# Kernel tuning notes

Measured on AMD Instinct MI355X. Metric: run time of the kernel, lower is better.

Reference implementation:

```python
import jax, jax.numpy as jnp
import numpy as np

PATCH = 4
WINDOW = 4
MAX_ROUNDS = 4
MIN_ROUNDS = 2
LAMBDA_P = 0.2
TOPK = 8


def _ln(x, g, b, eps=1e-5):
    m = x.mean(-1, keepdims=True)
    v = ((x - m) ** 2).mean(-1, keepdims=True)
    return (x - m) / jnp.sqrt(v + eps) * g + b


def _mlp(x, w1, b1, w2, b2):
    # Linear -> exact GELU -> Linear (matches nn.GELU default)
    return jax.nn.gelu(x @ w1 + b1, approximate=False) @ w2 + b2


def setup_inputs() -> dict:
    key = jax.random.key(0)
    ks = jax.random.split(key, 24)
    B, T, D, V = 16, 4096, 256, 256
    s = 0.02
    w = lambda i, shape: jax.random.normal(ks[i], shape, jnp.float32) * s
    z = lambda *shape: jnp.zeros(shape, jnp.float32)
    o = lambda *shape: jnp.ones(shape, jnp.float32)
    return {
        'x': jax.random.randint(ks[0], (B, T), 0, V),
        'emb': w(1, (V, D)), 'pos': w(2, (PATCH, D)),
        'gru_wih': w(3, (D, 3 * D)), 'gru_whh': w(4, (D, 3 * D)),
        'gru_bih': z(3 * D), 'gru_bhh': z(3 * D),
        'ln_p_g': o(D), 'ln_p_b': z(D),
        'sum_w': w(5, (D, D)), 'sum_b': z(D),
        'msg_w1': w(6, (2 * D, D)), 'msg_b1': z(D), 'msg_w2': w(7, (D, D)), 'msg_b2': z(D),
        'upd_w1': w(8, (2 * D, D)), 'upd_b1': z(D), 'upd_w2': w(9, (D, D)), 'upd_b2': z(D),
        'halt_w': w(10, (D, 1)), 'halt_b': z(1),
        'ln_mp_g': o(D), 'ln_mp_b': z(D),
        'q_w': w(11, (D, D)), 'q_b': z(D),
        'k_w': w(12, (D, D)), 'k_b': z(D),
        'v_w': w(13, (D, D)), 'v_b': z(D),
        'o_w': w(14, (D, D)), 'o_b': z(D),
        'bc_w': w(15, (D, D)), 'bc_b': z(D),
        'ln_f_g': o(D), 'ln_f_b': z(D),
        'head_w': w(16, (D, V)),
    }


def reference(x, emb, pos, gru_wih, gru_whh, gru_bih, gru_bhh, ln_p_g, ln_p_b,
              sum_w, sum_b, msg_w1, msg_b1, msg_w2, msg_b2, upd_w1, upd_b1,
              upd_w2, upd_b2, halt_w, halt_b, ln_mp_g, ln_mp_b, q_w, q_b,
              k_w, k_b, v_w, v_b, o_w, o_b, bc_w, bc_b, ln_f_g, ln_f_b, head_w):
    B, T = x.shape
    D = emb.shape[1]
    Np = T // PATCH  # T is divisible by PATCH for these shapes (no pad needed)

    # --- GRU patch processor over B*Np sequences of length PATCH ---
    tok = x.reshape(B * Np, PATCH)
    hseq = emb[tok] + pos[None]  # [BN, P, D]

    def gru_step(h, xt):
        gi = xt @ gru_wih + gru_bih
        gh = h @ gru_whh + gru_bhh
        ir, iz, inn = jnp.split(gi, 3, -1)
        hr, hz, hn = jnp.split(gh, 3, -1)
        r = jax.nn.sigmoid(ir + hr)
        zz = jax.nn.sigmoid(iz + hz)
        n = jnp.tanh(inn + r * hn)
        h = (1 - zz) * n + zz * h
        return h, h

    h0 = jnp.zeros((B * Np, D), hseq.dtype)
    _, gout = jax.lax.scan(gru_step, h0, jnp.swapaxes(hseq, 0, 1))
    local = _ln(jnp.swapaxes(gout, 0, 1), ln_p_g, ln_p_b).reshape(B, Np, PATCH, D)
    summaries = local.mean(2) @ sum_w + sum_b  # [B, Np, D]

    # --- Local message passing with ACT-style halting (fixed MAX_ROUNDS) ---
    h = summaries
    remaining = jnp.ones((B, Np, 1), h.dtype)
    out_mp = jnp.zeros_like(h)
    kl = jnp.zeros((), h.dtype)
    for step in range(MAX_ROUNDS):
        padded = jnp.pad(h, ((0, 0), (WINDOW, 0), (0, 0)))
        # neighbors: self plus previous WINDOW patches -> [B, Np, W+1, D]
        neigh = jnp.stack([padded[:, WINDOW - w:WINDOW - w + Np] for w in range(WINDOW + 1)], axis=2)
        self_exp = jnp.broadcast_to(h[:, :, None, :], neigh.shape)
        msgs = _mlp(jnp.concatenate([self_exp, neigh], -1), msg_w1, msg_b1, msg_w2, msg_b2).mean(2)
        h = _ln(h + _mlp(jnp.concatenate([h, msgs], -1), upd_w1, upd_b1, upd_w2, upd_b2), ln_mp_g, ln_mp_b)
        if step < MIN_ROUNDS:
            hp = jnp.zeros((B, Np, 1), h.dtype)
        else:
            hp = jax.nn.sigmoid(h.mean(1, keepdims=True) @ halt_w + halt_b)  # [B,1,1]
            hp = jnp.broadcast_to(hp, (B, Np, 1))
        if step == MAX_ROUNDS - 1:
            hp = jnp.ones_like(hp)
        out_mp = out_mp + remaining * hp * h
        remaining = remaining * (1 - hp)
        p_geom = LAMBDA_P * (1 - LAMBDA_P) ** step
        # F.kl_div(log(mean+eps), log(p_geom), log_target=True) = p*(log p - log(mean+eps))
        kl = kl + p_geom * (np.log(p_geom) - jnp.log(hp.mean() + 1e-8))
    kl = kl / MAX_ROUNDS

    # --- Sparse top-k causal retrieval ---
    q = out_mp @ q_w + q_b
    kk = out_mp @ k_w + k_b
    v = out_mp @ v_w + v_b
    scores = jnp.einsum('bnd,bmd->bnm', q, kk) / np.sqrt(D).astype(np.float32)
    causal = jnp.tril(jnp.ones((Np, Np), bool))
    neg = jnp.asarray(-jnp.inf, scores.dtype)
    scores = jnp.where(causal[None], scores, neg)
    vals, idx = jax.lax.top_k(scores, TOPK)  # [B, Np, k]
    bi = jnp.arange(B)[:, None, None]
    ni = jnp.arange(Np)[None, :, None]
    sparse = jnp.full_like(scores, neg).at[bi, ni, idx].set(vals)
    attn = jax.nn.softmax(sparse, axis=-1)
    retrieved = jnp.einsum('bnm,bmd->bnd', attn, v) @ o_w + o_b

    # --- Broadcast back to tokens and project ---
    combined = out_mp + retrieved
    broad = combined @ bc_w + bc_b
    final = (local + broad[:, :, None, :]).reshape(B, Np * PATCH, D)[:, :T]
    logits = _ln(final, ln_f_g, ln_f_b) @ head_w
    return logits, kl
```

## Files before the change

kernel.cpp:

```cpp
#include <hip/hip_runtime.h>
#include <math.h>


typedef __bf16 bf16_t;
typedef bf16_t bf16x8 __attribute__((ext_vector_type(8)));
typedef bf16_t bf16x4 __attribute__((ext_vector_type(4)));
typedef float f32x4 __attribute__((ext_vector_type(4)));

#define GF_BIAS 1
#define GF_GELU 4
#define GF_RES 8
#define GF_F32OUT 32

__device__ __forceinline__ float gelu_exact(float x) {
  return 0.5f * x * (1.0f + erff(x * 0.7071067811865475f));
}

__device__ __forceinline__ float sigm(float x) { return 1.f / (1.f + expf(-x)); }

__device__ __forceinline__ float wave_sum(float v) {
#pragma unroll
  for (int o = 32; o; o >>= 1) v += __shfl_xor(v, o, 64);
  return v;
}

__device__ __forceinline__ void gload16(const void* g, void* l) {
  __builtin_amdgcn_global_load_lds(
      (const __attribute__((address_space(1))) void*)g,
      (__attribute__((address_space(3))) void*)l, 16, 0, 0);
}

__device__ __forceinline__ unsigned long long skey(float s, int m) {
  unsigned u = __float_as_uint(s);
  u ^= (u & 0x80000000u) ? 0xFFFFFFFFu : 0x80000000u;
  return ((unsigned long long)u << 32) | (unsigned)(0x7FFFFFFF - m);
}

template<int FLAGS>
__global__ __launch_bounds__(256)
void gemm_bt(const bf16_t* __restrict__ A, const bf16_t* __restrict__ Bt,
             void* __restrict__ Cv, const float* __restrict__ bias,
             const bf16_t* __restrict__ res,
             int lda, int ldb, int ldc, int ldr)
{
  __shared__ __align__(16) bf16_t As[128][64];
  __shared__ __align__(16) bf16_t Bs[128][64];
  const int m0 = blockIdx.x * 128, n0 = blockIdx.y * 128;
  const int tid = threadIdx.x, lane = tid & 63, wave = tid >> 6;
  const int wm = (wave >> 1) << 6, wn = (wave & 1) << 6;
  const int lr = lane & 15, lg = lane >> 4;
  const int cx = lane & 7;

  const int srow = wave * 32 + (lane >> 3);
  const int scol = (((lane & 7) ^ ((lane >> 3) & 7)) * 8);
  const bf16_t* ga = A  + (long long)(m0 + srow) * lda + scol;
  const bf16_t* gb = Bt + (long long)(n0 + srow) * ldb + scol;
  char* lA = (char*)(&As[srow][0]) + (lane & 7) * 16;
  char* lB = (char*)(&Bs[srow][0]) + (lane & 7) * 16;

  f32x4 acc[4][4] = {};

#pragma unroll
  for (int kt = 0; kt < 4; kt++) {
    const int ko = kt * 64;
#pragma unroll
    for (int q = 0; q < 4; q++) {
      gload16(ga + (long long)q * 8 * lda + ko, lA + q * 1024);
      gload16(gb + (long long)q * 8 * ldb + ko, lB + q * 1024);
    }
    __syncthreads();
#pragma unroll
    for (int kk = 0; kk < 2; kk++) {
      const int co = ((kk * 4 + lg) ^ cx) << 4;
      bf16x8 af[4], bfv[4];
#pragma unroll
      for (int i = 0; i < 4; i++)
        af[i]  = *(const bf16x8*)((char*)As + (wm + i * 16 + lr) * 128 + co);
#pragma unroll
      for (int j = 0; j < 4; j++)
        bfv[j] = *(const bf16x8*)((char*)Bs + (wn + j * 16 + lr) * 128 + co);
#pragma unroll
      for (int i = 0; i < 4; i++)
#pragma unroll
        for (int j = 0; j < 4; j++)
          acc[i][j] = __builtin_amdgcn_mfma_f32_16x16x32_bf16(af[i], bfv[j], acc[i][j], 0, 0, 0);
    }
    if (kt < 3) __syncthreads();
  }

#pragma unroll
  for (int i = 0; i < 4; i++) {
#pragma unroll
    for (int j = 0; j < 4; j++) {
      const int col = n0 + wn + j * 16 + lr;
      const float bval = (FLAGS & GF_BIAS) ? bias[col] : 0.f;
#pragma unroll
      for (int e = 0; e < 4; e++) {
        const int row = m0 + wm + i * 16 + lg * 4 + e;
        float v = acc[i][j][e] + bval;
        if (FLAGS & GF_RES) v += (float)res[(long long)row * ldr + col];
        if (FLAGS & GF_GELU) v = gelu_exact(v);
        const long long ci = (long long)row * ldc + col;
        if (FLAGS & GF_F32OUT) ((float*)Cv)[ci] = v;
        else                   ((bf16_t*)Cv)[ci] = (bf16_t)v;
      }
    }
  }
}

template<int FLAGS>
__global__ __launch_bounds__(256)
void gemm64(const bf16_t* __restrict__ A, const bf16_t* __restrict__ Bt,
            void* __restrict__ Cv, const float* __restrict__ bias,
            const bf16_t* __restrict__ res,
            int lda, int ldb, int ldc, int ldr)
{
  __shared__ __align__(16) bf16_t As[64][64];
  __shared__ __align__(16) bf16_t Bs[64][64];
  const int m0 = blockIdx.x * 64, n0 = blockIdx.y * 64;
  const int tid = threadIdx.x, lane = tid & 63, wave = tid >> 6;
  const int wm = (wave >> 1) * 32, wn = (wave & 1) * 32;
  const int lr = lane & 15, lg = lane >> 4;
  const int cx = lane & 7;

  const int srow = tid >> 3;
  const int scol = (((tid & 7) ^ (srow & 7)) * 8);
  const bf16_t* ga = A  + (long long)(m0 + srow) * lda + scol;
  const bf16_t* gb = Bt + (long long)(n0 + srow) * ldb + scol;
  char* lA = (char*)As + tid * 16;
  char* lB = (char*)Bs + tid * 16;

  f32x4 acc[2][2] = {};

#pragma unroll
  for (int kt = 0; kt < 4; kt++) {
    const int ko = kt * 64;
    gload16(ga + ko, lA);
    gload16(ga + 32LL * lda + ko, lA + 4096);
    gload16(gb + ko, lB);
    gload16(gb + 32LL * ldb + ko, lB + 4096);
    __syncthreads();
#pragma unroll
    for (int kk = 0; kk < 2; kk++) {
      const int co = ((kk * 4 + lg) ^ cx) << 4;
      bf16x8 af[2], bfv[2];
#pragma unroll
      for (int i = 0; i < 2; i++)
        af[i]  = *(const bf16x8*)((char*)As + (wm + i * 16 + lr) * 128 + co);
#pragma unroll
      for (int j = 0; j < 2; j++)
        bfv[j] = *(const bf16x8*)((char*)Bs + (wn + j * 16 + lr) * 128 + co);
#pragma unroll
      for (int i = 0; i < 2; i++)
#pragma unroll
        for (int j = 0; j < 2; j++)
          acc[i][j] = __builtin_amdgcn_mfma_f32_16x16x32_bf16(af[i], bfv[j], acc[i][j], 0, 0, 0);
    }
    if (kt < 3) __syncthreads();
  }

#pragma unroll
  for (int i = 0; i < 2; i++) {
#pragma unroll
    for (int j = 0; j < 2; j++) {
      const int col = n0 + wn + j * 16 + lr;
      const float bval = (FLAGS & GF_BIAS) ? bias[col] : 0.f;
#pragma unroll
      for (int e = 0; e < 4; e++) {
        const int row = m0 + wm + i * 16 + lg * 4 + e;
        float v = acc[i][j][e] + bval;
        if (FLAGS & GF_RES) v += (float)res[(long long)row * ldr + col];
        if (FLAGS & GF_GELU) v = gelu_exact(v);
        const long long ci = (long long)row * ldc + col;
        if (FLAGS & GF_F32OUT) ((float*)Cv)[ci] = v;
        else                   ((bf16_t*)Cv)[ci] = (bf16_t)v;
      }
    }
  }
}

template<int MODE>
__global__ __launch_bounds__(256)
void gemm_ln(const bf16_t* __restrict__ A, const bf16_t* __restrict__ Bt,
             bf16_t* __restrict__ C, const float* __restrict__ bias,
             const float* __restrict__ g, const float* __restrict__ bvec,
             bf16_t* __restrict__ OUTMP, const float* __restrict__ HP)
{
  __shared__ __align__(16) bf16_t As[64][64];
  __shared__ __align__(16) bf16_t Bs[256][64];
  __shared__ float redsum[4][64];
  __shared__ float redsq[4][64];
  const int m0 = blockIdx.x * 64;
  const int tid = threadIdx.x, lane = tid & 63, w = tid >> 6;
  const int lr = lane & 15, lg = lane >> 4, cx = lane & 7;

  f32x4 acc[4][4] = {};

#pragma unroll
  for (int kt = 0; kt < 4; kt++) {
    const int ko = kt * 64;
    {
      int cid = tid, r = cid >> 3, c = cid & 7;
      gload16(A + (long long)(m0 + r) * 256 + ko + ((c ^ (r & 7)) * 8), (char*)As + cid * 16);
      cid = tid + 256; r = cid >> 3; c = cid & 7;
      gload16(A + (long long)(m0 + r) * 256 + ko + ((c ^ (r & 7)) * 8), (char*)As + cid * 16);
    }
#pragma unroll
    for (int it = 0; it < 8; it++) {
      const int cid = it * 256 + tid, r = cid >> 3, c = cid & 7;
      gload16(Bt + (long long)r * 256 + ko + ((c ^ (r & 7)) * 8), (char*)Bs + cid * 16);
    }
    __syncthreads();
#pragma unroll
    for (int kk = 0; kk < 2; kk++) {
      const int co = ((kk * 4 + lg) ^ cx) << 4;
      bf16x8 af[4], bfv[4];
#pragma unroll
      for (int i = 0; i < 4; i++)
        af[i]  = *(const bf16x8*)((char*)As + (i * 16 + lr) * 128 + co);
#pragma unroll
      for (int j = 0; j < 4; j++)
        bfv[j] = *(const bf16x8*)((char*)Bs + (w * 64 + j * 16 + lr) * 128 + co);
#pragma unroll
      for (int i = 0; i < 4; i++)
#pragma unroll
        for (int j = 0; j < 4; j++)
          acc[i][j] = __builtin_amdgcn_mfma_f32_16x16x32_bf16(af[i], bfv[j], acc[i][j], 0, 0, 0);
    }
    if (kt < 3) __syncthreads();
  }

  float v[4][4][4];
  float rs[4][4], rq[4][4];
#pragma unroll
  for (int i = 0; i < 4; i++) {
#pragma unroll
    for (int e = 0; e < 4; e++) { rs[i][e] = 0.f; rq[i][e] = 0.f; }
  }
#pragma unroll
  for (int i = 0; i < 4; i++) {
#pragma unroll
    for (int j = 0; j < 4; j++) {
      const int col = w * 64 + j * 16 + lr;
      const float bval = bias[col];
#pragma unroll
      for (int e = 0; e < 4; e++) {
        const long long rg = m0 + i * 16 + lg * 4 + e;
        const float val = acc[i][j][e] + bval + (float)C[rg * 256 + col];
        v[i][j][e] = val;
        rs[i][e] += val;
        rq[i][e] += val * val;
      }
    }
  }
#pragma unroll
  for (int off = 1; off < 16; off <<= 1) {
#pragma unroll
    for (int i = 0; i < 4; i++)
#pragma unroll
      for (int e = 0; e < 4; e++) {
        rs[i][e] += __shfl_xor(rs[i][e], off, 64);
        rq[i][e] += __shfl_xor(rq[i][e], off, 64);
      }
  }
  if (lr == 0) {
#pragma unroll
    for (int i = 0; i < 4; i++)
#pragma unroll
      for (int e = 0; e < 4; e++) {
        redsum[w][i * 16 + lg * 4 + e] = rs[i][e];
        redsq[w][i * 16 + lg * 4 + e]  = rq[i][e];
      }
  }
  __syncthreads();
  float mean[4][4], rstd[4][4];
#pragma unroll
  for (int i = 0; i < 4; i++) {
#pragma unroll
    for (int e = 0; e < 4; e++) {
      const int r = i * 16 + lg * 4 + e;
      const float S = redsum[0][r] + redsum[1][r] + redsum[2][r] + redsum[3][r];
      const float Q = redsq[0][r] + redsq[1][r] + redsq[2][r] + redsq[3][r];
      const float m = S * (1.f / 256.f);
      float var = Q * (1.f / 256.f) - m * m;
      if (var < 0.f) var = 0.f;
      mean[i][e] = m;
      rstd[i][e] = rsqrtf(var + 1e-5f);
    }
  }
#pragma unroll
  for (int i = 0; i < 4; i++) {
#pragma unroll
    for (int j = 0; j < 4; j++) {
      const int col = w * 64 + j * 16 + lr;
      const float gg = g[col], bb = bvec[col];
#pragma unroll
      for (int e = 0; e < 4; e++) {
        const long long rg = m0 + i * 16 + lg * 4 + e;
        const float y = (v[i][j][e] - mean[i][e]) * rstd[i][e] * gg + bb;
        if (MODE == 0) {
          C[rg * 256 + col] = (bf16_t)y;
        } else {
          const float rem = 1.f - HP[(int)(rg >> 10)];
          OUTMP[rg * 256 + col] = (bf16_t)((float)OUTMP[rg * 256 + col] + rem * y);
        }
      }
    }
  }
}

__global__ __launch_bounds__(256)
void k_fatopk(const bf16_t* __restrict__ QKV, bf16_t* __restrict__ O) {
  __shared__ unsigned long long cand[4][16][8];
  __shared__ float wrow[16][8];
  __shared__ int   irow[16][8];
  const int b = blockIdx.y;
  const int tid = threadIdx.x;
  const int wid = tid >> 6;
  const int lane = tid & 63;
  const int lr = lane & 15, lg = lane >> 4;
  const bf16_t* Qp = QKV + (long long)b * (1024LL * 768);
  const bf16_t* Kp = Qp + 256;
  const bf16_t* Vp = Qp + 512;

  for (int half = 0; half < 2; half++) {
    const int qw = (half == 0) ? (int)blockIdx.x : 63 - (int)blockIdx.x;
    const int q0 = qw * 16;
    const int qrow = q0 + lr;

    bf16x8 bq[8];
#pragma unroll
    for (int s = 0; s < 8; s++)
      bq[s] = *(const bf16x8*)(Qp + (long long)qrow * 768 + s * 32 + lg * 8);

    unsigned long long kv[8] = {0ull, 0ull, 0ull, 0ull, 0ull, 0ull, 0ull, 0ull};

#define INS8(KEY) {                                                     \
    const unsigned long long k_ = (KEY);                                \
    if (k_ > kv[7]) {                                                   \
      kv[7] = k_;                                                       \
      _Pragma("unroll")                                                 \
      for (int j_ = 7; j_ > 0; j_--)                                    \
        if (kv[j_] > kv[j_-1]) {                                        \
          const unsigned long long t_ = kv[j_];                         \
          kv[j_] = kv[j_-1]; kv[j_-1] = t_;                             \
        }                                                               \
    }                                                                   \
  }

    const int klim = qw + 1;
    for (int kt = wid; kt < klim; kt += 4) {
      const bf16_t* ka = Kp + (long long)(kt * 16 + lr) * 768 + lg * 8;
      bf16x8 af[8];
#pragma unroll
      for (int s = 0; s < 8; s++) af[s] = *(const bf16x8*)(ka + s * 32);
      f32x4 a0 = {}, a1 = {};
#pragma unroll
      for (int s = 0; s < 8; s += 2) {
        a0 = __builtin_amdgcn_mfma_f32_16x16x32_bf16(af[s],     bq[s],     a0, 0, 0, 0);
        a1 = __builtin_amdgcn_mfma_f32_16x16x32_bf16(af[s + 1], bq[s + 1], a1, 0, 0, 0);
      }
#pragma unroll
      for (int e = 0; e < 4; e++) {
        const int m = kt * 16 + lg * 4 + e;
        if (m <= qrow) INS8(skey((a0[e] + a1[e]) * 0.0625f, m));
      }
    }
#undef INS8

#pragma unroll
    for (int r = 0; r < 8; r++) {
      unsigned long long mk = kv[0];
      unsigned long long ok = __shfl_xor(mk, 16, 64); if (ok > mk) mk = ok;
      ok = __shfl_xor(mk, 32, 64); if (ok > mk) mk = ok;
      if (lg == 0) cand[wid][lr][r] = mk;
      if (kv[0] == mk && mk != 0ull) {
#pragma unroll
        for (int j = 0; j < 7; j++) kv[j] = kv[j + 1];
        kv[7] = 0ull;
      }
    }
    __syncthreads();

    if (wid == 0) {
      unsigned long long kv2[8];
#pragma unroll
      for (int j = 0; j < 8; j++) kv2[j] = cand[lg][lr][j];
      float wv[8]; int wi[8];
#pragma unroll
      for (int r = 0; r < 8; r++) {
        unsigned long long mk = kv2[0];
        unsigned long long ok = __shfl_xor(mk, 16, 64); if (ok > mk) mk = ok;
        ok = __shfl_xor(mk, 32, 64); if (ok > mk) mk = ok;
        if (mk != 0ull) {
          unsigned hi = (unsigned)(mk >> 32);
          hi ^= (hi & 0x80000000u) ? 0x80000000u : 0xFFFFFFFFu;
          wv[r] = __uint_as_float(hi);
          wi[r] = 0x7FFFFFFF - (int)(unsigned)(mk & 0xFFFFFFFFu);
        } else {
          wv[r] = 0.f; wi[r] = -1;
        }
        if (kv2[0] == mk && mk != 0ull) {
#pragma unroll
          for (int j = 0; j < 7; j++) kv2[j] = kv2[j + 1];
          kv2[7] = 0ull;
        }
      }
      const float mx = wv[0];
      float w8[8]; float den = 0.f;
#pragma unroll
      for (int j = 0; j < 8; j++) {
        w8[j] = (wi[j] >= 0) ? expf(wv[j] - mx) : 0.f;
        den += w8[j];
      }
      const float inv = 1.f / den;
      if (lg == 0) {
#pragma unroll
        for (int j = 0; j < 8; j++) {
          wrow[lr][j] = w8[j] * inv;
          irow[lr][j] = wi[j];
        }
      }
    }
    __syncthreads();

    const int rr = wid * 4 + lg;
    const int c0 = (lane & 15) * 16;
    f32x4 av[4] = {};
#pragma unroll
    for (int j = 0; j < 8; j++) {
      const int idx = irow[rr][j];
      if (idx >= 0) {
        const float wj = wrow[rr][j];
        const bf16_t* vr = Vp + (long long)idx * 768 + c0;
        const bf16x8 v0 = *(const bf16x8*)vr;
        const bf16x8 v1 = *(const bf16x8*)(vr + 8);
#pragma unroll
        for (int e = 0; e < 4; e++) {
          av[0][e] = fmaf(wj, (float)v0[e],     av[0][e]);
          av[1][e] = fmaf(wj, (float)v0[4 + e], av[1][e]);
          av[2][e] = fmaf(wj, (float)v1[e],     av[2][e]);
          av[3][e] = fmaf(wj, (float)v1[4 + e], av[3][e]);
        }
      }
    }
    bf16_t* op = O + ((long long)b * 1024 + q0 + rr) * 256 + c0;
    bf16x8 o0, o1;
#pragma unroll
    for (int e = 0; e < 4; e++) {
      o0[e] = (bf16_t)av[0][e]; o0[4 + e] = (bf16_t)av[1][e];
      o1[e] = (bf16_t)av[2][e]; o1[4 + e] = (bf16_t)av[3][e];
    }
    *(bf16x8*)op = o0;
    *(bf16x8*)(op + 8) = o1;
    if (half == 0) __syncthreads();
  }
}

struct TD { const float* src; bf16_t* dst; int N; int k0; int ld; };
struct PrepArgs {
  TD d[16];
  const float* emb; const float* pos; bf16_t* XE;
  const float* msg_b1; const float* msg_b2; const float* upd_w1; const float* upd_b1;
  const float* q_b; const float* k_b; const float* v_b;
  float* BIAS3; float* QKVB;
};

__global__ __launch_bounds__(256) void k_prep(PrepArgs pa) {
  const int y = blockIdx.y, x = blockIdx.x, d = threadIdx.x;
  if (y < 16) {
    TD t = pa.d[y];
    if (x >= t.N) return;
    if (t.k0 < 0) t.dst[(long long)x * 256 + d] = (bf16_t)t.src[(long long)x * t.ld + d];
    else          t.dst[(long long)x * 256 + d] = (bf16_t)t.src[(long long)(t.k0 + d) * t.ld + x];
  } else if (y == 16) {
    const int p = x >> 8, v = x & 255;
    pa.XE[(long long)x * 256 + d] = (bf16_t)(pa.emb[v * 256 + d] + pa.pos[p * 256 + d]);
  } else {
    if      (x == 0) pa.BIAS3[d] = pa.msg_b1[d];
    else if (x == 1) pa.BIAS3[256 + d] = 0.f;
    else if (x == 2) {
      float acc = pa.upd_b1[d];
      for (int k = 0; k < 256; k++) acc += pa.msg_b2[k] * pa.upd_w1[(long long)(256 + k) * 256 + d];
      pa.BIAS3[512 + d] = acc;
    }
    else if (x == 3) pa.QKVB[d] = pa.q_b[d];
    else if (x == 4) pa.QKVB[256 + d] = pa.k_b[d];
    else if (x == 5) pa.QKVB[512 + d] = pa.v_b[d];
  }
}

__global__ __launch_bounds__(64)
void k_gru_gate(const int* __restrict__ x, const bf16_t* __restrict__ gitab,
                const bf16_t* __restrict__ GH, const float* __restrict__ bhh,
                bf16_t* __restrict__ H, bf16_t* __restrict__ LOC, int t)
{
  const int s = blockIdx.x, lane = threadIdx.x, d0 = lane * 4;
  const int v = x[s * 4 + t];
  const bf16_t* gi = gitab + (long long)(t * 256 + v) * 768;
  const bf16x4 g_r = *(const bf16x4*)(gi + d0);
  const bf16x4 g_z = *(const bf16x4*)(gi + 256 + d0);
  const bf16x4 g_n = *(const bf16x4*)(gi + 512 + d0);
  float hr[4], hz[4], hn[4], hp[4];
  if (t == 0) {
#pragma unroll
    for (int e = 0; e < 4; e++) {
      hr[e] = bhh[d0 + e]; hz[e] = bhh[256 + d0 + e]; hn[e] = bhh[512 + d0 + e];
      hp[e] = 0.f;
    }
  } else {
    const bf16_t* gh = GH + (long long)s * 768;
    const bf16x4 a = *(const bf16x4*)(gh + d0);
    const bf16x4 b4 = *(const bf16x4*)(gh + 256 + d0);
    const bf16x4 c4 = *(const bf16x4*)(gh + 512 + d0);
    const bf16x4 hv = *(const bf16x4*)(H + (long long)s * 256 + d0);
#pragma unroll
    for (int e = 0; e < 4; e++) { hr[e] = a[e]; hz[e] = b4[e]; hn[e] = c4[e]; hp[e] = hv[e]; }
  }
  bf16x4 ho;
#pragma unroll
  for (int e = 0; e < 4; e++) {
    const float r = sigm((float)g_r[e] + hr[e]);
    const float zz = sigm((float)g_z[e] + hz[e]);
    const float nn = tanhf((float)g_n[e] + r * hn[e]);
    ho[e] = (bf16_t)((1.f - zz) * nn + zz * hp[e]);
  }
  *(bf16x4*)(H + (long long)s * 256 + d0) = ho;
  *(bf16x4*)(LOC + ((long long)s * 4 + t) * 256 + d0) = ho;
}

__global__ __launch_bounds__(64)
void k_ln(const bf16_t* __restrict__ X, const bf16_t* __restrict__ ADD, int addmode,
          bf16_t* __restrict__ OUT, const float* __restrict__ g,
          const float* __restrict__ b)
{
  const long long r = blockIdx.x;
  const int d0 = threadIdx.x * 4;
  const bf16x4 xv = *(const bf16x4*)(X + r * 256 + d0);
  float xf[4];
#pragma unroll
  for (int e = 0; e < 4; e++) xf[e] = (float)xv[e];
  if (addmode == 1) {
    const bf16x4 av = *(const bf16x4*)(ADD + r * 256 + d0);
#pragma unroll
    for (int e = 0; e < 4; e++) xf[e] += (float)av[e];
  } else if (addmode == 2) {
    const bf16x4 av = *(const bf16x4*)(ADD + (r >> 2) * 256 + d0);
#pragma unroll
    for (int e = 0; e < 4; e++) xf[e] += (float)av[e];
  }
  const float mean = wave_sum(xf[0] + xf[1] + xf[2] + xf[3]) * (1.f / 256.f);
  float q = 0.f;
#pragma unroll
  for (int e = 0; e < 4; e++) { const float dx = xf[e] - mean; q += dx * dx; }
  const float rstd = rsqrtf(wave_sum(q) * (1.f / 256.f) + 1e-5f);
  const float4 gv = *(const float4*)(g + d0);
  const float4 bv = *(const float4*)(b + d0);
  const float gg[4] = {gv.x, gv.y, gv.z, gv.w};
  const float bb[4] = {bv.x, bv.y, bv.z, bv.w};
  bf16x4 ov;
#pragma unroll
  for (int e = 0; e < 4; e++) ov[e] = (bf16_t)((xf[e] - mean) * rstd * gg[e] + bb[e]);
  *(bf16x4*)(OUT + r * 256 + d0) = ov;
}

__global__ __launch_bounds__(64)
void k_lnp4(bf16_t* __restrict__ LOC, bf16_t* __restrict__ SUMB,
            const float* __restrict__ g, const float* __restrict__ b)
{
  const long long s = blockIdx.x;
  const int d0 = threadIdx.x * 4;
  const float4 gv = *(const float4*)(g + d0);
  const float4 bv = *(const float4*)(b + d0);
  const float gg[4] = {gv.x, gv.y, gv.z, gv.w};
  const float bb[4] = {bv.x, bv.y, bv.z, bv.w};
  float accd[4] = {0.f, 0.f, 0.f, 0.f};
#pragma unroll
  for (int t = 0; t < 4; t++) {
    bf16_t* row = LOC + (s * 4 + t) * 256 + d0;
    const bf16x4 xv = *(const bf16x4*)row;
    float xf[4];
#pragma unroll
    for (int e = 0; e < 4; e++) xf[e] = (float)xv[e];
    const float mean = wave_sum(xf[0] + xf[1] + xf[2] + xf[3]) * (1.f / 256.f);
    float q = 0.f;
#pragma unroll
    for (int e = 0; e < 4; e++) { const float dx = xf[e] - mean; q += dx * dx; }
    const float rstd = rsqrtf(wave_sum(q) * (1.f / 256.f) + 1e-5f);
    bf16x4 ov;
#pragma unroll
    for (int e = 0; e < 4; e++) {
      const float y = (xf[e] - mean) * rstd * gg[e] + bb[e];
      ov[e] = (bf16_t)y;
      accd[e] += y;
    }
    *(bf16x4*)row = ov;
  }
  bf16x4 sv;
#pragma unroll
  for (int e = 0; e < 4; e++) sv[e] = (bf16_t)(accd[e] * 0.25f);
  *(bf16x4*)(SUMB + s * 256 + d0) = sv;
}

__global__ __launch_bounds__(64)
void k_gelumix(const bf16_t* __restrict__ A3, bf16_t* __restrict__ G)
{
  const long long s = blockIdx.x;
  const int n = (int)(s & 1023);
  const int d0 = threadIdx.x * 4;
  const bf16x4 av = *(const bf16x4*)(A3 + s * 768 + d0);
  float a[4];
#pragma unroll
  for (int e = 0; e < 4; e++) a[e] = (float)av[e];
  float acc[4] = {0.f, 0.f, 0.f, 0.f};
  const bf16_t* bbase = A3 + s * 768 + 256 + d0;
#pragma unroll
  for (int w = 0; w <= 4; w++) {
    if (n >= w) {
      const bf16x4 bn = *(const bf16x4*)(bbase - (long long)w * 768);
#pragma unroll
      for (int e = 0; e < 4; e++) acc[e] += gelu_exact(a[e] + (float)bn[e]);
    } else {
#pragma unroll
      for (int e = 0; e < 4; e++) acc[e] += gelu_exact(a[e]);
    }
  }
  bf16x4 ov;
#pragma unroll
  for (int e = 0; e < 4; e++) ov[e] = (bf16_t)(acc[e] * 0.2f);
  *(bf16x4*)(G + s * 256 + d0) = ov;
}

__global__ __launch_bounds__(64)
void k_halt1(const bf16_t* __restrict__ Hm, float* __restrict__ PS) {
  const int c = blockIdx.x, b = blockIdx.y, d0 = threadIdx.x * 4;
  float acc[4] = {0.f, 0.f, 0.f, 0.f};
  const bf16_t* base = Hm + ((long long)b * 1024 + c * 32) * 256 + d0;
#pragma unroll 4
  for (int n = 0; n < 32; n++) {
    const bf16x4 hv = *(const bf16x4*)(base + (long long)n * 256);
#pragma unroll
    for (int e = 0; e < 4; e++) acc[e] += (float)hv[e];
  }
  float4 o4; o4.x = acc[0]; o4.y = acc[1]; o4.z = acc[2]; o4.w = acc[3];
  *(float4*)(PS + ((long long)b * 32 + c) * 256 + d0) = o4;
}

__global__ __launch_bounds__(1024)
void k_halt2kl(const float* __restrict__ PS, const float* __restrict__ hw,
               const float* __restrict__ hb, float* __restrict__ HP,
               float* __restrict__ out) {
  __shared__ float sh[16];
  const int b = threadIdx.x >> 6, lane = threadIdx.x & 63, d0 = lane * 4;
  float acc[4] = {0.f, 0.f, 0.f, 0.f};
  for (int c = 0; c < 32; c++) {
    const float4 p4 = *(const float4*)(PS + ((long long)b * 32 + c) * 256 + d0);
    acc[0] += p4.x; acc[1] += p4.y; acc[2] += p4.z; acc[3] += p4.w;
  }
  const float4 w4 = *(const float4*)(hw + d0);
  float val = (acc[0] * w4.x + acc[1] * w4.y + acc[2] * w4.z + acc[3] * w4.w) * (1.f / 1024.f);
  val = wave_sum(val);
  if (lane == 0) {
    const float hp = sigm(val + hb[0]);
    HP[b] = hp;
    sh[b] = hp;
  }
  __syncthreads();
  if (threadIdx.x == 0) {
    float s = 0.f;
    for (int bb = 0; bb < 16; bb++) s += sh[bb];
    const float hpm = s * (1.f / 16.f);
    const float l8 = logf(1e-8f);
    const float p0 = 0.2f, p1 = 0.16f, p2 = 0.128f, p3 = 0.1024f;
    const float kl = p0 * (logf(p0) - l8)
                   + p1 * (logf(p1) - l8)
                   + p2 * (logf(p2) - logf(hpm + 1e-8f))
                   + p3 * (logf(p3) - logf(1.f + 1e-8f));
    out[0] = kl * 0.25f;
  }
}

__global__ __launch_bounds__(64)
void k_outmp(const bf16_t* __restrict__ Hm, const float* __restrict__ HP,
             bf16_t* __restrict__ O, int acc) {
  const long long s = blockIdx.x;
  const int d0 = threadIdx.x * 4;
  const int b = (int)(s >> 10);
  const float hp = HP[b];
  const bf16x4 hv = *(const bf16x4*)(Hm + s * 256 + d0);
  bf16x4 ov;
  if (acc) {
    const bf16x4 pv = *(const bf16x4*)(O + s * 256 + d0);
#pragma unroll
    for (int e = 0; e < 4; e++) ov[e] = (bf16_t)((float)pv[e] + (1.f - hp) * (float)hv[e]);
  } else {
#pragma unroll
    for (int e = 0; e < 4; e++) ov[e] = (bf16_t)(hp * (float)hv[e]);
  }
  *(bf16x4*)(O + s * 256 + d0) = ov;
}

extern "C" void kernel_launch(void* const* d_in, const int* in_sizes, int n_in,
                              void* d_out, int out_size, void* d_ws, size_t ws_size,
                              hipStream_t stream) {
  (void)in_sizes; (void)n_in; (void)ws_size;
  const int*   x      = (const int*)d_in[0];
  const float* emb    = (const float*)d_in[1];
  const float* pos    = (const float*)d_in[2];
  const float* wih    = (const float*)d_in[3];
  const float* whh    = (const float*)d_in[4];
  const float* bih    = (const float*)d_in[5];
  const float* bhh    = (const float*)d_in[6];
  const float* lnp_g  = (const float*)d_in[7];
  const float* lnp_b  = (const float*)d_in[8];
  const float* sum_w  = (const float*)d_in[9];
  const float* sum_b  = (const float*)d_in[10];
  const float* msg_w1 = (const float*)d_in[11];
  const float* msg_b1 = (const float*)d_in[12];
  const float* msg_w2 = (const float*)d_in[13];
  const float* msg_b2 = (const float*)d_in[14];
  const float* upd_w1 = (const float*)d_in[15];
  const float* upd_b1 = (const float*)d_in[16];
  const float* upd_w2 = (const float*)d_in[17];
  const float* upd_b2 = (const float*)d_in[18];
  const float* halt_w = (const float*)d_in[19];
  const float* halt_b = (const float*)d_in[20];
  const float* lnm_g  = (const float*)d_in[21];
  const float* lnm_b  = (const float*)d_in[22];
  const float* q_b    = (const float*)d_in[24];
  const float* k_b    = (const float*)d_in[26];
  const float* v_b    = (const float*)d_in[28];
  const float* o_b    = (const float*)d_in[30];
  const float* bc_b   = (const float*)d_in[32];
  const float* lnf_g  = (const float*)d_in[33];
  const float* lnf_b  = (const float*)d_in[34];

  char* base = (char*)d_ws;
  size_t off = 0;
  auto alloc = [&](size_t bytes) -> void* {
    void* p = (void*)(base + off);
    off += (bytes + 255) & ~(size_t)255;
    return p;
  };
  const size_t SL2 = 16384ull * 256 * 2;
  bf16_t* WIHT  = (bf16_t*)alloc(768 * 256 * 2);
  bf16_t* WHHT  = (bf16_t*)alloc(768 * 256 * 2);
  bf16_t* SUMT  = (bf16_t*)alloc(256 * 256 * 2);
  bf16_t* MW    = (bf16_t*)alloc(768 * 256 * 2);
  bf16_t* W2T   = (bf16_t*)alloc(256 * 256 * 2);
  bf16_t* W2NT  = (bf16_t*)alloc(256 * 256 * 2);
  bf16_t* UW1MT = (bf16_t*)alloc(256 * 256 * 2);
  bf16_t* UW2T  = (bf16_t*)alloc(256 * 256 * 2);
  bf16_t* WCB   = (bf16_t*)alloc(256 * 256 * 2);
  bf16_t* QKVW  = (bf16_t*)alloc(768 * 256 * 2);
  bf16_t* OT    = (bf16_t*)alloc(256 * 256 * 2);
  bf16_t* BCT   = (bf16_t*)alloc(256 * 256 * 2);
  bf16_t* HEADT = (bf16_t*)alloc(256 * 256 * 2);
  float*  BIAS3 = (float*)alloc(768 * 4);
  float*  QKVB  = (float*)alloc(768 * 4);
  bf16_t* XE    = (bf16_t*)alloc(1024ull * 256 * 2);
  bf16_t* GITAB = (bf16_t*)alloc(1024ull * 768 * 2);
  bf16_t* LOCb  = (bf16_t*)alloc(65536ull * 256 * 2);

  char*   SCR   = (char*)alloc(16ull * 1024 * 1024 * 4);
  bf16_t* GH    = (bf16_t*)SCR;
  bf16_t* H     = (bf16_t*)(SCR + 25165824);
  bf16_t* SUMB  = (bf16_t*)(SCR + 33554432);
  bf16_t* A3    = (bf16_t*)(SCR + 41943040);

  bf16_t* HMP   = (bf16_t*)alloc(SL2);
  bf16_t* G     = (bf16_t*)alloc(SL2);
  bf16_t* BROAD = (bf16_t*)alloc(SL2);
  bf16_t* UB    = (bf16_t*)alloc(SL2);
  bf16_t* U2B   = (bf16_t*)alloc(SL2);
  bf16_t* OUTMP = (bf16_t*)alloc(SL2);
  bf16_t* QKV   = (bf16_t*)alloc(16384ull * 768 * 2);
  float*  PS    = (float*)alloc(512ull * 256 * 4);
  float*  HP    = (float*)alloc(64);
  bf16_t* ATT   = UB;
  bf16_t* COMB  = U2B;
  float*  out   = (float*)d_out;
  float*  klout = out + (out_size - 1);

  PrepArgs pa;
  pa.d[0]  = { wih,                    WIHT,            768, 0,   768 };
  pa.d[1]  = { whh,                    WHHT,            768, 0,   768 };
  pa.d[2]  = { sum_w,                  SUMT,            256, 0,   256 };
  pa.d[3]  = { msg_w1,                 MW,              256, 0,   256 };
  pa.d[4]  = { msg_w1,                 MW + 256 * 256,  256, 256, 256 };
  pa.d[5]  = { upd_w1,                 MW + 512 * 256,  256, 0,   256 };
  pa.d[6]  = { msg_w2,                 W2T,             256, 0,   256 };
  pa.d[7]  = { upd_w1,                 UW1MT,           256, 256, 256 };
  pa.d[8]  = { upd_w2,                 UW2T,            256, 0,   256 };
  pa.d[9]  = { (const float*)d_in[23], QKVW,            256, 0,   256 };
  pa.d[10] = { (const float*)d_in[25], QKVW + 256*256,  256, 0,   256 };
  pa.d[11] = { (const float*)d_in[27], QKVW + 512*256,  256, 0,   256 };
  pa.d[12] = { (const float*)d_in[29], OT,              256, 0,   256 };
  pa.d[13] = { (const float*)d_in[31], BCT,             256, 0,   256 };
  pa.d[14] = { (const float*)d_in[35], HEADT,           256, 0,   256 };
  pa.d[15] = { msg_w2,                 W2NT,            256, -1,  256 };
  pa.emb = emb; pa.pos = pos; pa.XE = XE;
  pa.msg_b1 = msg_b1; pa.msg_b2 = msg_b2; pa.upd_w1 = upd_w1; pa.upd_b1 = upd_b1;
  pa.q_b = q_b; pa.k_b = k_b; pa.v_b = v_b;
  pa.BIAS3 = BIAS3; pa.QKVB = QKVB;
  k_prep<<<dim3(1024, 18), 256, 0, stream>>>(pa);

  gemm64<0><<<dim3(4, 4), 256, 0, stream>>>(
      UW1MT, W2NT, WCB, nullptr, nullptr, 256, 256, 256, 0);

  gemm64<GF_BIAS><<<dim3(16, 12), 256, 0, stream>>>(
      XE, WIHT, GITAB, bih, nullptr, 256, 256, 768, 0);

  k_gru_gate<<<16384, 64, 0, stream>>>(x, GITAB, GH, bhh, H, LOCb, 0);
  for (int t = 1; t < 4; t++) {
    gemm_bt<GF_BIAS><<<dim3(128, 6), 256, 0, stream>>>(
        H, WHHT, GH, bhh, nullptr, 256, 256, 768, 0);
    k_gru_gate<<<16384, 64, 0, stream>>>(x, GITAB, GH, bhh, H, LOCb, t);
  }

  k_lnp4<<<16384, 64, 0, stream>>>(LOCb, SUMB, lnp_g, lnp_b);
  gemm64<GF_BIAS><<<dim3(256, 4), 256, 0, stream>>>(
      SUMB, SUMT, HMP, sum_b, nullptr, 256, 256, 256, 0);

  for (int step = 0; step < 4; step++) {
    gemm_bt<GF_BIAS><<<dim3(128, 6), 256, 0, stream>>>(
        HMP, MW, A3, BIAS3, nullptr, 256, 256, 768, 0);
    k_gelumix<<<16384, 64, 0, stream>>>(A3, G);
    gemm64<GF_RES | GF_GELU><<<dim3(256, 4), 256, 0, stream>>>(
        G, WCB, UB, nullptr, A3 + 512, 256, 256, 256, 768);
    if (step == 3) {
      gemm_ln<1><<<256, 256, 0, stream>>>(
          UB, UW2T, HMP, upd_b2, lnm_g, lnm_b, OUTMP, HP);
    } else {
      gemm_ln<0><<<256, 256, 0, stream>>>(
          UB, UW2T, HMP, upd_b2, lnm_g, lnm_b, nullptr, nullptr);
      if (step == 2) {
        k_halt1<<<dim3(32, 16), 64, 0, stream>>>(HMP, PS);
        k_halt2kl<<<1, 1024, 0, stream>>>(PS, halt_w, halt_b, HP, klout);
        k_outmp<<<16384, 64, 0, stream>>>(HMP, HP, OUTMP, 0);
      }
    }
  }

  gemm_bt<GF_BIAS><<<dim3(128, 6), 256, 0, stream>>>(
      OUTMP, QKVW, QKV, QKVB, nullptr, 256, 256, 768, 0);
  k_fatopk<<<dim3(32, 16), 256, 0, stream>>>(QKV, ATT);
  gemm64<GF_BIAS | GF_RES><<<dim3(256, 4), 256, 0, stream>>>(
      ATT, OT, COMB, o_b, OUTMP, 256, 256, 256, 256);
  gemm64<GF_BIAS><<<dim3(256, 4), 256, 0, stream>>>(
      COMB, BCT, BROAD, bc_b, nullptr, 256, 256, 256, 0);

  k_ln<<<65536, 64, 0, stream>>>(LOCb, BROAD, 2, LOCb, lnf_g, lnf_b);
  gemm_bt<GF_F32OUT><<<dim3(512, 2), 256, 0, stream>>>(
      LOCb, HEADT, out, nullptr, nullptr, 256, 256, 256, 0);
}
```

Before: 470.2 us.

## Split topk blocks per query tile, pair key tiles, pack rows per block

```diff
diff --git a/kernel.cpp b/kernel.cpp
--- a/kernel.cpp
+++ b/kernel.cpp
@@ -315,6 +315,7 @@
   __shared__ float wrow[16][8];
   __shared__ int   irow[16][8];
   const int b = blockIdx.y;
+  const int qw = (int)((blockIdx.x + ((unsigned)(b * 21) & 63u)) & 63u);
   const int tid = threadIdx.x;
   const int wid = tid >> 6;
   const int lane = tid & 63;
@@ -322,18 +323,15 @@
   const bf16_t* Qp = QKV + (long long)b * (1024LL * 768);
   const bf16_t* Kp = Qp + 256;
   const bf16_t* Vp = Qp + 512;
-
-  for (int half = 0; half < 2; half++) {
-    const int qw = (half == 0) ? (int)blockIdx.x : 63 - (int)blockIdx.x;
-    const int q0 = qw * 16;
-    const int qrow = q0 + lr;
-
-    bf16x8 bq[8];
-#pragma unroll
-    for (int s = 0; s < 8; s++)
-      bq[s] = *(const bf16x8*)(Qp + (long long)qrow * 768 + s * 32 + lg * 8);
-
-    unsigned long long kv[8] = {0ull, 0ull, 0ull, 0ull, 0ull, 0ull, 0ull, 0ull};
+  const int q0 = qw * 16;
+  const int qrow = q0 + lr;
+
+  bf16x8 bq[8];
+#pragma unroll
+  for (int s = 0; s < 8; s++)
+    bq[s] = *(const bf16x8*)(Qp + (long long)qrow * 768 + s * 32 + lg * 8);
+
+  unsigned long long kv[8] = {0ull, 0ull, 0ull, 0ull, 0ull, 0ull, 0ull, 0ull};
 
 #define INS8(KEY) {                                                     \
     const unsigned long long k_ = (KEY);                                \
@@ -348,113 +346,127 @@
     }                                                                   \
   }
 
-    const int klim = qw + 1;
-    for (int kt = wid; kt < klim; kt += 4) {
-      const bf16_t* ka = Kp + (long long)(kt * 16 + lr) * 768 + lg * 8;
-      bf16x8 af[8];
-#pragma unroll
-      for (int s = 0; s < 8; s++) af[s] = *(const bf16x8*)(ka + s * 32);
-      f32x4 a0 = {}, a1 = {};
-#pragma unroll
-      for (int s = 0; s < 8; s += 2) {
-        a0 = __builtin_amdgcn_mfma_f32_16x16x32_bf16(af[s],     bq[s],     a0, 0, 0, 0);
-        a1 = __builtin_amdgcn_mfma_f32_16x16x32_bf16(af[s + 1], bq[s + 1], a1, 0, 0, 0);
-      }
+  const int klim = qw + 1;
+  for (int base = wid * 2; base < klim; base += 8) {
+    const bool hasB = (base + 1 < klim);
+    const int ktB = hasB ? base + 1 : base;
+    const bf16_t* ka = Kp + (long long)(base * 16 + lr) * 768 + lg * 8;
+    const bf16_t* kb = Kp + (long long)(ktB * 16 + lr) * 768 + lg * 8;
+    bf16x8 afA[8], afB[8];
+#pragma unroll
+    for (int s = 0; s < 8; s++) afA[s] = *(const bf16x8*)(ka + s * 32);
+#pragma unroll
+    for (int s = 0; s < 8; s++) afB[s] = *(const bf16x8*)(kb + s * 32);
+    f32x4 a0 = {}, a1 = {}, b0 = {}, b1 = {};
+    __builtin_amdgcn_s_setprio(1);
+#pragma unroll
+    for (int s = 0; s < 8; s += 2) {
+      a0 = __builtin_amdgcn_mfma_f32_16x16x32_bf16(afA[s],     bq[s],     a0, 0, 0, 0);
+      a1 = __builtin_amdgcn_mfma_f32_16x16x32_bf16(afA[s + 1], bq[s + 1], a1, 0, 0, 0);
+      b0 = __builtin_amdgcn_mfma_f32_16x16x32_bf16(afB[s],     bq[s],     b0, 0, 0, 0);
+      b1 = __builtin_amdgcn_mfma_f32_16x16x32_bf16(afB[s + 1], bq[s + 1], b1, 0, 0, 0);
+    }
+    __builtin_amdgcn_s_setprio(0);
+#pragma unroll
+    for (int e = 0; e < 4; e++) {
+      const int m = base * 16 + lg * 4 + e;
+      if (m <= qrow) INS8(skey((a0[e] + a1[e]) * 0.0625f, m));
+    }
+    if (hasB) {
 #pragma unroll
       for (int e = 0; e < 4; e++) {
-        const int m = kt * 16 + lg * 4 + e;
-        if (m <= qrow) INS8(skey((a0[e] + a1[e]) * 0.0625f, m));
-      }
-    }
+        const int m = ktB * 16 + lg * 4 + e;
+        if (m <= qrow) INS8(skey((b0[e] + b1[e]) * 0.0625f, m));
+      }
+    }
+  }
 #undef INS8
 
 #pragma unroll
+  for (int r = 0; r < 8; r++) {
+    unsigned long long mk = kv[0];
+    unsigned long long ok = __shfl_xor(mk, 16, 64); if (ok > mk) mk = ok;
+    ok = __shfl_xor(mk, 32, 64); if (ok > mk) mk = ok;
+    if (lg == 0) cand[wid][lr][r] = mk;
+    if (kv[0] == mk && mk != 0ull) {
+#pragma unroll
+      for (int j = 0; j < 7; j++) kv[j] = kv[j + 1];
+      kv[7] = 0ull;
+    }
+  }
+  __syncthreads();
+
+  if (wid == 0) {
+    unsigned long long kv2[8];
+#pragma unroll
+    for (int j = 0; j < 8; j++) kv2[j] = cand[lg][lr][j];
+    float wv[8]; int wi[8];
+#pragma unroll
     for (int r = 0; r < 8; r++) {
-      unsigned long long mk = kv[0];
+      unsigned long long mk = kv2[0];
       unsigned long long ok = __shfl_xor(mk, 16, 64); if (ok > mk) mk = ok;
       ok = __shfl_xor(mk, 32, 64); if (ok > mk) mk = ok;
-      if (lg == 0) cand[wid][lr][r] = mk;
-      if (kv[0] == mk && mk != 0ull) {
-#pragma unroll
-        for (int j = 0; j < 7; j++) kv[j] = kv[j + 1];
-        kv[7] = 0ull;
-      }
-    }
-    __syncthreads();
-
-    if (wid == 0) {
-      unsigned long long kv2[8];
-#pragma unroll
-      for (int j = 0; j < 8; j++) kv2[j] = cand[lg][lr][j];
-      float wv[8]; int wi[8];
-#pragma unroll
-      for (int r = 0; r < 8; r++) {
-        unsigned long long mk = kv2[0];
-        unsigned long long ok = __shfl_xor(mk, 16, 64); if (ok > mk) mk = ok;
-        ok = __shfl_xor(mk, 32, 64); if (ok > mk) mk = ok;
-        if (mk != 0ull) {
-          unsigned hi = (unsigned)(mk >> 32);
-          hi ^= (hi & 0x80000000u) ? 0x80000000u : 0xFFFFFFFFu;
-          wv[r] = __uint_as_float(hi);
-          wi[r] = 0x7FFFFFFF - (int)(unsigned)(mk & 0xFFFFFFFFu);
-        } else {
-          wv[r] = 0.f; wi[r] = -1;
-        }
-        if (kv2[0] == mk && mk != 0ull) {
-#pragma unroll
-          for (int j = 0; j < 7; j++) kv2[j] = kv2[j + 1];
-          kv2[7] = 0ull;
-        }
-      }
-      const float mx = wv[0];
-      float w8[8]; float den = 0.f;
+      if (mk != 0ull) {
+        unsigned hi = (unsigned)(mk >> 32);
+        hi ^= (hi & 0x80000000u) ? 0x80000000u : 0xFFFFFFFFu;
+        wv[r] = __uint_as_float(hi);
+        wi[r] = 0x7FFFFFFF - (int)(unsigned)(mk & 0xFFFFFFFFu);
+      } else {
+        wv[r] = 0.f; wi[r] = -1;
+      }
+      if (kv2[0] == mk && mk != 0ull) {
+#pragma unroll
+        for (int j = 0; j < 7; j++) kv2[j] = kv2[j + 1];
+        kv2[7] = 0ull;
+      }
+    }
+    const float mx = wv[0];
+    float w8[8]; float den = 0.f;
+#pragma unroll
+    for (int j = 0; j < 8; j++) {
+      w8[j] = (wi[j] >= 0) ? expf(wv[j] - mx) : 0.f;
+      den += w8[j];
+    }
+    const float inv = 1.f / den;
+    if (lg == 0) {
 #pragma unroll
       for (int j = 0; j < 8; j++) {
-        w8[j] = (wi[j] >= 0) ? expf(wv[j] - mx) : 0.f;
-        den += w8[j];
-      }
-      const float inv = 1.f / den;
-      if (lg == 0) {
-#pragma unroll
-        for (int j = 0; j < 8; j++) {
-          wrow[lr][j] = w8[j] * inv;
-          irow[lr][j] = wi[j];
-        }
-      }
-    }
-    __syncthreads();
-
-    const int rr = wid * 4 + lg;
-    const int c0 = (lane & 15) * 16;
-    f32x4 av[4] = {};
-#pragma unroll
-    for (int j = 0; j < 8; j++) {
-      const int idx = irow[rr][j];
-      if (idx >= 0) {
-        const float wj = wrow[rr][j];
-        const bf16_t* vr = Vp + (long long)idx * 768 + c0;
-        const bf16x8 v0 = *(const bf16x8*)vr;
-        const bf16x8 v1 = *(const bf16x8*)(vr + 8);
-#pragma unroll
-        for (int e = 0; e < 4; e++) {
-          av[0][e] = fmaf(wj, (float)v0[e],     av[0][e]);
-          av[1][e] = fmaf(wj, (float)v0[4 + e], av[1][e]);
-          av[2][e] = fmaf(wj, (float)v1[e],     av[2][e]);
-          av[3][e] = fmaf(wj, (float)v1[4 + e], av[3][e]);
-        }
-      }
-    }
-    bf16_t* op = O + ((long long)b * 1024 + q0 + rr) * 256 + c0;
-    bf16x8 o0, o1;
-#pragma unroll
-    for (int e = 0; e < 4; e++) {
-      o0[e] = (bf16_t)av[0][e]; o0[4 + e] = (bf16_t)av[1][e];
-      o1[e] = (bf16_t)av[2][e]; o1[4 + e] = (bf16_t)av[3][e];
-    }
-    *(bf16x8*)op = o0;
-    *(bf16x8*)(op + 8) = o1;
-    if (half == 0) __syncthreads();
-  }
+        wrow[lr][j] = w8[j] * inv;
+        irow[lr][j] = wi[j];
+      }
+    }
+  }
+  __syncthreads();
+
+  const int rr = wid * 4 + lg;
+  const int c0 = (lane & 15) * 16;
+  f32x4 av[4] = {};
+#pragma unroll
+  for (int j = 0; j < 8; j++) {
+    const int idx = irow[rr][j];
+    if (idx >= 0) {
+      const float wj = wrow[rr][j];
+      const bf16_t* vr = Vp + (long long)idx * 768 + c0;
+      const bf16x8 v0 = *(const bf16x8*)vr;
+      const bf16x8 v1 = *(const bf16x8*)(vr + 8);
+#pragma unroll
+      for (int e = 0; e < 4; e++) {
+        av[0][e] = fmaf(wj, (float)v0[e],     av[0][e]);
+        av[1][e] = fmaf(wj, (float)v0[4 + e], av[1][e]);
+        av[2][e] = fmaf(wj, (float)v1[e],     av[2][e]);
+        av[3][e] = fmaf(wj, (float)v1[4 + e], av[3][e]);
+      }
+    }
+  }
+  bf16_t* op = O + ((long long)b * 1024 + q0 + rr) * 256 + c0;
+  bf16x8 o0, o1;
+#pragma unroll
+  for (int e = 0; e < 4; e++) {
+    o0[e] = (bf16_t)av[0][e]; o0[4 + e] = (bf16_t)av[1][e];
+    o1[e] = (bf16_t)av[2][e]; o1[4 + e] = (bf16_t)av[3][e];
+  }
+  *(bf16x8*)op = o0;
+  *(bf16x8*)(op + 8) = o1;
 }
 
 struct TD { const float* src; bf16_t* dst; int N; int k0; int ld; };
@@ -490,12 +502,13 @@
   }
 }
 
-__global__ __launch_bounds__(64)
+__global__ __launch_bounds__(256)
 void k_gru_gate(const int* __restrict__ x, const bf16_t* __restrict__ gitab,
                 const bf16_t* __restrict__ GH, const float* __restrict__ bhh,
                 bf16_t* __restrict__ H, bf16_t* __restrict__ LOC, int t)
 {
-  const int s = blockIdx.x, lane = threadIdx.x, d0 = lane * 4;
+  const int s = blockIdx.x * 4 + (threadIdx.x >> 6);
+  const int lane = threadIdx.x & 63, d0 = lane * 4;
   const int v = x[s * 4 + t];
   const bf16_t* gi = gitab + (long long)(t * 256 + v) * 768;
   const bf16x4 g_r = *(const bf16x4*)(gi + d0);
@@ -529,13 +542,13 @@
   *(bf16x4*)(LOC + ((long long)s * 4 + t) * 256 + d0) = ho;
 }
 
-__global__ __launch_bounds__(64)
+__global__ __launch_bounds__(256)
 void k_ln(const bf16_t* __restrict__ X, const bf16_t* __restrict__ ADD, int addmode,
           bf16_t* __restrict__ OUT, const float* __restrict__ g,
           const float* __restrict__ b)
 {
-  const long long r = blockIdx.x;
-  const int d0 = threadIdx.x * 4;
+  const long long r = (long long)blockIdx.x * 4 + (threadIdx.x >> 6);
+  const int d0 = (threadIdx.x & 63) * 4;
   const bf16x4 xv = *(const bf16x4*)(X + r * 256 + d0);
   float xf[4];
 #pragma unroll
@@ -564,12 +577,12 @@
   *(bf16x4*)(OUT + r * 256 + d0) = ov;
 }
 
-__global__ __launch_bounds__(64)
+__global__ __launch_bounds__(256)
 void k_lnp4(bf16_t* __restrict__ LOC, bf16_t* __restrict__ SUMB,
             const float* __restrict__ g, const float* __restrict__ b)
 {
-  const long long s = blockIdx.x;
-  const int d0 = threadIdx.x * 4;
+  const long long s = (long long)blockIdx.x * 4 + (threadIdx.x >> 6);
+  const int d0 = (threadIdx.x & 63) * 4;
   const float4 gv = *(const float4*)(g + d0);
   const float4 bv = *(const float4*)(b + d0);
   const float gg[4] = {gv.x, gv.y, gv.z, gv.w};
@@ -602,12 +615,12 @@
   *(bf16x4*)(SUMB + s * 256 + d0) = sv;
 }
 
-__global__ __launch_bounds__(64)
+__global__ __launch_bounds__(256)
 void k_gelumix(const bf16_t* __restrict__ A3, bf16_t* __restrict__ G)
 {
-  const long long s = blockIdx.x;
+  const long long s = (long long)blockIdx.x * 4 + (threadIdx.x >> 6);
   const int n = (int)(s & 1023);
-  const int d0 = threadIdx.x * 4;
+  const int d0 = (threadIdx.x & 63) * 4;
   const bf16x4 av = *(const bf16x4*)(A3 + s * 768 + d0);
   float a[4];
 #pragma unroll
@@ -680,23 +693,17 @@
   }
 }
 
-__global__ __launch_bounds__(64)
+__global__ __launch_bounds__(256)
 void k_outmp(const bf16_t* __restrict__ Hm, const float* __restrict__ HP,
-             bf16_t* __restrict__ O, int acc) {
-  const long long s = blockIdx.x;
-  const int d0 = threadIdx.x * 4;
+             bf16_t* __restrict__ O) {
+  const long long s = (long long)blockIdx.x * 4 + (threadIdx.x >> 6);
+  const int d0 = (threadIdx.x & 63) * 4;
   const int b = (int)(s >> 10);
   const float hp = HP[b];
   const bf16x4 hv = *(const bf16x4*)(Hm + s * 256 + d0);
   bf16x4 ov;
-  if (acc) {
-    const bf16x4 pv = *(const bf16x4*)(O + s * 256 + d0);
-#pragma unroll
-    for (int e = 0; e < 4; e++) ov[e] = (bf16_t)((float)pv[e] + (1.f - hp) * (float)hv[e]);
-  } else {
-#pragma unroll
-    for (int e = 0; e < 4; e++) ov[e] = (bf16_t)(hp * (float)hv[e]);
-  }
+#pragma unroll
+  for (int e = 0; e < 4; e++) ov[e] = (bf16_t)(hp * (float)hv[e]);
   *(bf16x4*)(O + s * 256 + d0) = ov;
 }
 
@@ -811,21 +818,21 @@
   gemm64<GF_BIAS><<<dim3(16, 12), 256, 0, stream>>>(
       XE, WIHT, GITAB, bih, nullptr, 256, 256, 768, 0);
 
-  k_gru_gate<<<16384, 64, 0, stream>>>(x, GITAB, GH, bhh, H, LOCb, 0);
+  k_gru_gate<<<4096, 256, 0, stream>>>(x, GITAB, GH, bhh, H, LOCb, 0);
   for (int t = 1; t < 4; t++) {
     gemm_bt<GF_BIAS><<<dim3(128, 6), 256, 0, stream>>>(
         H, WHHT, GH, bhh, nullptr, 256, 256, 768, 0);
-    k_gru_gate<<<16384, 64, 0, stream>>>(x, GITAB, GH, bhh, H, LOCb, t);
-  }
-
-  k_lnp4<<<16384, 64, 0, stream>>>(LOCb, SUMB, lnp_g, lnp_b);
+    k_gru_gate<<<4096, 256, 0, stream>>>(x, GITAB, GH, bhh, H, LOCb, t);
+  }
+
+  k_lnp4<<<4096, 256, 0, stream>>>(LOCb, SUMB, lnp_g, lnp_b);
   gemm64<GF_BIAS><<<dim3(256, 4), 256, 0, stream>>>(
       SUMB, SUMT, HMP, sum_b, nullptr, 256, 256, 256, 0);
 
   for (int step = 0; step < 4; step++) {
     gemm_bt<GF_BIAS><<<dim3(128, 6), 256, 0, stream>>>(
         HMP, MW, A3, BIAS3, nullptr, 256, 256, 768, 0);
-    k_gelumix<<<16384, 64, 0, stream>>>(A3, G);
+    k_gelumix<<<4096, 256, 0, stream>>>(A3, G);
     gemm64<GF_RES | GF_GELU><<<dim3(256, 4), 256, 0, stream>>>(
         G, WCB, UB, nullptr, A3 + 512, 256, 256, 256, 768);
     if (step == 3) {
@@ -837,20 +844,20 @@
       if (step == 2) {
         k_halt1<<<dim3(32, 16), 64, 0, stream>>>(HMP, PS);
         k_halt2kl<<<1, 1024, 0, stream>>>(PS, halt_w, halt_b, HP, klout);
-        k_outmp<<<16384, 64, 0, stream>>>(HMP, HP, OUTMP, 0);
+        k_outmp<<<4096, 256, 0, stream>>>(HMP, HP, OUTMP);
       }
     }
   }
 
   gemm_bt<GF_BIAS><<<dim3(128, 6), 256, 0, stream>>>(
       OUTMP, QKVW, QKV, QKVB, nullptr, 256, 256, 768, 0);
-  k_fatopk<<<dim3(32, 16), 256, 0, stream>>>(QKV, ATT);
+  k_fatopk<<<dim3(64, 16), 256, 0, stream>>>(QKV, ATT);
   gemm64<GF_BIAS | GF_RES><<<dim3(256, 4), 256, 0, stream>>>(
       ATT, OT, COMB, o_b, OUTMP, 256, 256, 256, 256);
   gemm64<GF_BIAS><<<dim3(256, 4), 256, 0, stream>>>(
       COMB, BCT, BROAD, bc_b, nullptr, 256, 256, 256, 0);
 
-  k_ln<<<65536, 64, 0, stream>>>(LOCb, BROAD, 2, LOCb, lnf_g, lnf_b);
+  k_ln<<<16384, 256, 0, stream>>>(LOCb, BROAD, 2, LOCb, lnf_g, lnf_b);
   gemm_bt<GF_F32OUT><<<dim3(512, 2), 256, 0, stream>>>(
       LOCb, HEADT, out, nullptr, nullptr, 256, 256, 256, 0);
 }
```

Measured after the change: 466.7 us. Within noise of the previous version (-0.8%).
